# Optimization experiments

Measured on AMD Instinct MI355X. Metric: run time of the kernel, lower is better.

Reference implementation:

```python
import jax, jax.numpy as jnp
import numpy as np

B, T, F, U, H = 4096, 64, 128, 256, 256
MC_STEPS = 32
DENOISE = True


def setup_inputs() -> dict:
    key = jax.random.key(0)
    ks = jax.random.split(key, 12)
    su = 1.0 / np.sqrt(U)
    inp = {
        "x": jax.random.normal(ks[0], (B, T, F), jnp.float32),
        # LSTM params (torch gate order i,f,g,o)
        "W_ih": jax.random.uniform(ks[1], (4 * U, F), jnp.float32, -su, su),
        "W_hh": jax.random.uniform(ks[2], (4 * U, U), jnp.float32, -su, su),
        "b_ih": jax.random.uniform(ks[3], (4 * U,), jnp.float32, -su, su),
        "b_hh": jax.random.uniform(ks[4], (4 * U,), jnp.float32, -su, su),
        # CRBM conditioning nets: bias (ny), precision (ny), weights (ny*nh)
        "bias_W": jax.random.normal(ks[5], (F, U), jnp.float32) * su,
        "bias_b": jnp.zeros((F,), jnp.float32),
        "prec_W": jax.random.normal(ks[6], (F, U), jnp.float32) * su,
        "prec_b": jnp.zeros((F,), jnp.float32),
        "wts_W": jax.random.normal(ks[7], (F * H, U), jnp.float32) * su,
        "wts_b": jnp.zeros((F * H,), jnp.float32),
    }
    return inp


def _lstm_last_hidden(x, W_ih, W_hh, b_ih, b_hh):
    # single-layer batch_first LSTM; returns last hidden state [B, U]
    b, u = x.shape[0], W_hh.shape[1]
    bias = b_ih + b_hh

    def step(carry, xt):
        h, c = carry
        g = xt @ W_ih.T + h @ W_hh.T + bias          # [B, 4U]
        i, f, gg, o = jnp.split(g, 4, axis=-1)
        c = jax.nn.sigmoid(f) * c + jax.nn.sigmoid(i) * jnp.tanh(gg)
        h = jax.nn.sigmoid(o) * jnp.tanh(c)
        return (h, c), None

    h0 = jnp.zeros((b, u), x.dtype)
    (h, _), _ = jax.lax.scan(step, (h0, h0), jnp.swapaxes(x, 0, 1))
    return h


def _crbm_sample(xh, bias_W, bias_b, prec_W, prec_b, wts_W, wts_b,
                 mc_steps=MC_STEPS, denoise=DENOISE):
    b = xh.shape[0]
    bias = xh @ bias_W.T + bias_b                              # [B, F]
    precision = jax.nn.softplus(xh @ prec_W.T + prec_b) + 1e-6  # [B, F] > 0
    weights = (xh @ wts_W.T + wts_b).reshape(b, F, H)           # [B, F, H]
    std = jax.lax.rsqrt(precision)

    key = jax.random.key(1)
    k0, kloop = jax.random.split(key)
    y0 = bias + std * jax.random.normal(k0, bias.shape, bias.dtype)

    def gibbs(y, k):
        kh, ky = jax.random.split(k)
        h_prob = jax.nn.sigmoid(jnp.einsum("bf,bfh->bh", y, weights))
        h = (jax.random.uniform(kh, h_prob.shape) < h_prob).astype(y.dtype)
        mean = bias + jnp.einsum("bfh,bh->bf", weights, h) / precision
        y = mean + std * jax.random.normal(ky, mean.shape, mean.dtype)
        return y, mean

    y_last, means = jax.lax.scan(gibbs, y0, jax.random.split(kloop, mc_steps))
    y_model = means[-1] if denoise else y_last
    return y_model, bias, precision, weights


def reference(x, W_ih, W_hh, b_ih, b_hh, bias_W, bias_b, prec_W, prec_b, wts_W, wts_b):
    xh = _lstm_last_hidden(x, W_ih, W_hh, b_ih, b_hh)
    y_model, _, _, _ = _crbm_sample(xh, bias_W, bias_b, prec_W, prec_b, wts_W, wts_b)
    return y_model
```

## Files before the change

kernel.cpp:

```cpp
#include <hip/hip_runtime.h>
#include <stdint.h>

#pragma clang fp contract(off)

#define B 4096
#define T 64
#define F 128
#define U 256
#define H 256
#define GU 1024
#define NJ 32768
#define MC 32
#define CH 256
#define BT 32

__host__ __device__ inline void tf2x32(uint32_t k0, uint32_t k1,
                                       uint32_t x0, uint32_t x1,
                                       uint32_t& o0, uint32_t& o1) {
  uint32_t ks2 = k0 ^ k1 ^ 0x1BD11BDAu;
  x0 += k0; x1 += k1;
#define TFR(r) { x0 += x1; x1 = (x1 << r) | (x1 >> (32 - r)); x1 ^= x0; }
  TFR(13) TFR(15) TFR(26) TFR(6)
  x0 += k1;  x1 += ks2 + 1u;
  TFR(17) TFR(29) TFR(16) TFR(24)
  x0 += ks2; x1 += k0 + 2u;
  TFR(13) TFR(15) TFR(26) TFR(6)
  x0 += k0;  x1 += k1 + 3u;
  TFR(17) TFR(29) TFR(16) TFR(24)
  x0 += k1;  x1 += ks2 + 4u;
  TFR(13) TFR(15) TFR(26) TFR(6)
  x0 += ks2; x1 += k0 + 5u;
#undef TFR
  o0 = x0; o1 = x1;
}

__device__ inline uint32_t tf_bits(uint32_t kx, uint32_t ky, uint32_t i) {
  uint32_t o0, o1;
  tf2x32(kx, ky, 0u, i, o0, o1);
  return o0 ^ o1;
}

__device__ inline float u01_f32(uint32_t bits) {
  return __uint_as_float((bits >> 9) | 0x3F800000u) - 1.0f;
}

__device__ inline float erfinv_f32(float x) {
  float w = -log1pf(-(x * x));
  float p;
  if (w < 5.0f) {
    float ww = w - 2.5f;
    p = 2.81022636e-08f;
    p = p * ww + 3.43273939e-07f;
    p = p * ww + (-3.5233877e-06f);
    p = p * ww + (-4.39150654e-06f);
    p = p * ww + 0.00021858087f;
    p = p * ww + (-0.00125372503f);
    p = p * ww + (-0.00417768164f);
    p = p * ww + 0.246640727f;
    p = p * ww + 1.50140941f;
  } else {
    float ww = sqrtf(w) - 3.0f;
    p = -0.000200214257f;
    p = p * ww + 0.000100950558f;
    p = p * ww + 0.00134934322f;
    p = p * ww + (-0.00367342844f);
    p = p * ww + 0.00573950773f;
    p = p * ww + (-0.0076224613f);
    p = p * ww + 0.00943887047f;
    p = p * ww + 1.00167406f;
    p = p * ww + 2.83297682f;
  }
  return p * x;
}

__device__ inline float normal_f32(uint32_t kx, uint32_t ky, uint32_t i) {
  float f = u01_f32(tf_bits(kx, ky, i));
  const float lo = -0.99999994039535522461f;
  float v = f * 2.0f + lo;
  v = fmaxf(lo, v);
  return 1.4142135623730951f * erfinv_f32(v);
}

__device__ inline float sigmoid_f32(float x) {
  return 1.0f / (1.0f + expf(-x));
}
__device__ inline float softplus_f32(float x) {
  return fmaxf(x, 0.0f) + log1pf(expf(-fabsf(x)));
}

__global__ void prep_lstm_w_k(const float* __restrict__ W_ih, const float* __restrict__ W_hh,
                              const float* __restrict__ b_ih, const float* __restrict__ b_hh,
                              float4* __restrict__ w4t, float* __restrict__ biasg) {
  int idx = blockIdx.x * 256 + threadIdx.x;
  if (idx < GU * 96) {
    int j = idx / 96, k4 = idx - j * 96;
    float v[4];
#pragma unroll
    for (int m = 0; m < 4; ++m) {
      int k = k4 * 4 + m;
      v[m] = (k < F) ? W_ih[(size_t)j * F + k] : W_hh[(size_t)j * U + (k - F)];
    }
    w4t[(size_t)k4 * GU + j] = make_float4(v[0], v[1], v[2], v[3]);
  }
  if (idx < GU) biasg[idx] = b_ih[idx] + b_hh[idx];
}

__global__ void prep_wts_k(const float* __restrict__ wts_W, float4* __restrict__ wts4t) {
  int idx = blockIdx.x * 256 + threadIdx.x;
  if (idx >= NJ * 64) return;
  int j = idx >> 6, k4 = idx & 63;
  const float* r = wts_W + (size_t)j * U + k4 * 4;
  wts4t[(size_t)k4 * NJ + j] = make_float4(r[0], r[1], r[2], r[3]);
}

__global__ void prep_bp_k(const float* __restrict__ bias_W, const float* __restrict__ prec_W,
                          float4* __restrict__ bp4t) {
  int idx = blockIdx.x * 256 + threadIdx.x;
  if (idx >= 256 * 64) return;
  int j = idx >> 6, k4 = idx & 63;
  const float* r = (j < F) ? (bias_W + (size_t)j * U + k4 * 4)
                           : (prec_W + (size_t)(j - F) * U + k4 * 4);
  bp4t[(size_t)k4 * 256 + j] = make_float4(r[0], r[1], r[2], r[3]);
}

__global__ __launch_bounds__(256) void lstm_step_k(
    const float* __restrict__ x, const float* __restrict__ h_in,
    const float* __restrict__ c_in, const float4* __restrict__ w4t,
    const float* __restrict__ biasg, float* __restrict__ h_out,
    float* __restrict__ c_out, int t) {
  __shared__ __align__(16) float xt[BT * 128];
  __shared__ __align__(16) float ht[BT * 256];
  const int tid = threadIdx.x;
  const int b0 = blockIdx.x * BT;
  const int ut = blockIdx.y;
  for (int q = tid; q < BT * 32; q += 256) {
    int row = q >> 5, c4 = q & 31;
    *(float4*)(xt + row * 128 + c4 * 4) =
        *(const float4*)(x + ((size_t)(b0 + row) * T + t) * F + c4 * 4);
  }
  for (int q = tid; q < BT * 64; q += 256) {
    int row = q >> 6, c4 = q & 63;
    *(float4*)(ht + row * 256 + c4 * 4) =
        *(const float4*)(h_in + (size_t)(b0 + row) * U + c4 * 4);
  }
  __syncthreads();
  const int u_loc = tid & 63, bg = tid >> 6;
  const int u = ut * 64 + u_loc;
  float accX[4][8], accH[4][8];
#pragma unroll
  for (int g = 0; g < 4; ++g)
#pragma unroll
    for (int b = 0; b < 8; ++b) { accX[g][b] = 0.0f; accH[g][b] = 0.0f; }

#pragma unroll 4
  for (int k4 = 0; k4 < 32; ++k4) {
    float4 wf[4];
#pragma unroll
    for (int g = 0; g < 4; ++g) wf[g] = w4t[(size_t)k4 * GU + g * U + u];
#pragma unroll
    for (int b = 0; b < 8; ++b) {
      float4 av = *(const float4*)(xt + (bg * 8 + b) * 128 + k4 * 4);
#pragma unroll
      for (int g = 0; g < 4; ++g) {
        accX[g][b] = fmaf(av.x, wf[g].x, accX[g][b]);
        accX[g][b] = fmaf(av.y, wf[g].y, accX[g][b]);
        accX[g][b] = fmaf(av.z, wf[g].z, accX[g][b]);
        accX[g][b] = fmaf(av.w, wf[g].w, accX[g][b]);
      }
    }
  }
#pragma unroll 4
  for (int k4 = 32; k4 < 96; ++k4) {
    float4 wf[4];
#pragma unroll
    for (int g = 0; g < 4; ++g) wf[g] = w4t[(size_t)k4 * GU + g * U + u];
#pragma unroll
    for (int b = 0; b < 8; ++b) {
      float4 av = *(const float4*)(ht + (bg * 8 + b) * 256 + (k4 - 32) * 4);
#pragma unroll
      for (int g = 0; g < 4; ++g) {
        accH[g][b] = fmaf(av.x, wf[g].x, accH[g][b]);
        accH[g][b] = fmaf(av.y, wf[g].y, accH[g][b]);
        accH[g][b] = fmaf(av.z, wf[g].z, accH[g][b]);
        accH[g][b] = fmaf(av.w, wf[g].w, accH[g][b]);
      }
    }
  }
  float bi = biasg[u], bf = biasg[U + u], bgg = biasg[2 * U + u], bo = biasg[3 * U + u];
#pragma unroll
  for (int b = 0; b < 8; ++b) {
    size_t gi = (size_t)(b0 + bg * 8 + b) * U + u;
    float c = c_in[gi];
    float g_i = (accX[0][b] + accH[0][b]) + bi;
    float g_f = (accX[1][b] + accH[1][b]) + bf;
    float g_g = (accX[2][b] + accH[2][b]) + bgg;
    float g_o = (accX[3][b] + accH[3][b]) + bo;
    float t1 = sigmoid_f32(g_f) * c;
    float t2 = sigmoid_f32(g_i) * tanhf(g_g);
    float cn = t1 + t2;
    float hn = sigmoid_f32(g_o) * tanhf(cn);
    c_out[gi] = cn;
    h_out[gi] = hn;
  }
}

__global__ __launch_bounds__(256) void gemm_xh_k(
    const float* __restrict__ xh_c, const float4* __restrict__ wts4t,
    const float* __restrict__ wts_b, float* __restrict__ outp) {
  __shared__ __align__(16) float xl[64 * 256];
  const int tid = threadIdx.x;
  const int b0 = blockIdx.x * 64;
  const int j = blockIdx.y * 256 + tid;
  for (int q = tid; q < 64 * 64; q += 256) {
    int row = q >> 6, c4 = q & 63;
    *(float4*)(xl + row * 256 + c4 * 4) =
        *(const float4*)(xh_c + (size_t)(b0 + row) * U + c4 * 4);
  }
  __syncthreads();
  float acc[64];
#pragma unroll
  for (int b = 0; b < 64; ++b) acc[b] = 0.0f;
  for (int k4 = 0; k4 < 64; ++k4) {
    float4 wf = wts4t[(size_t)k4 * NJ + j];
#pragma unroll
    for (int b = 0; b < 64; ++b) {
      float4 av = *(const float4*)(xl + b * 256 + k4 * 4);
      acc[b] = fmaf(av.x, wf.x, acc[b]);
      acc[b] = fmaf(av.y, wf.y, acc[b]);
      acc[b] = fmaf(av.z, wf.z, acc[b]);
      acc[b] = fmaf(av.w, wf.w, acc[b]);
    }
  }
  float bb = wts_b[j];
#pragma unroll
  for (int b = 0; b < 64; ++b)
    outp[(size_t)(b0 + b) * NJ + j] = acc[b] + bb;
}

__global__ __launch_bounds__(256) void biasprec_k(
    const float* __restrict__ xh, const float4* __restrict__ bp4t,
    const float* __restrict__ bias_b, const float* __restrict__ prec_b,
    float* __restrict__ bias_g, float* __restrict__ prec_g) {
  __shared__ __align__(16) float xl[64 * 256];
  const int tid = threadIdx.x;
  const int b0 = blockIdx.x * 64;
  const int j = tid;
  for (int q = tid; q < 64 * 64; q += 256) {
    int row = q >> 6, c4 = q & 63;
    *(float4*)(xl + row * 256 + c4 * 4) =
        *(const float4*)(xh + (size_t)(b0 + row) * U + c4 * 4);
  }
  __syncthreads();
  float acc[64];
#pragma unroll
  for (int b = 0; b < 64; ++b) acc[b] = 0.0f;
  for (int k4 = 0; k4 < 64; ++k4) {
    float4 wf = bp4t[(size_t)k4 * 256 + j];
#pragma unroll
    for (int b = 0; b < 64; ++b) {
      float4 av = *(const float4*)(xl + b * 256 + k4 * 4);
      acc[b] = fmaf(av.x, wf.x, acc[b]);
      acc[b] = fmaf(av.y, wf.y, acc[b]);
      acc[b] = fmaf(av.z, wf.z, acc[b]);
      acc[b] = fmaf(av.w, wf.w, acc[b]);
    }
  }
  if (j < F) {
    float bb = bias_b[j];
#pragma unroll
    for (int b = 0; b < 64; ++b)
      bias_g[(size_t)(b0 + b) * F + j] = acc[b] + bb;
  } else {
    float pb = prec_b[j - F];
#pragma unroll
    for (int b = 0; b < 64; ++b)
      prec_g[(size_t)(b0 + b) * F + (j - F)] = softplus_f32(acc[b] + pb) + 1e-6f;
  }
}

struct GKeys {
  uint32_t k0x, k0y;
  uint32_t khx[32], khy[32], kyx[32], kyy[32];
};

__global__ __launch_bounds__(256) void gibbs_k(
    const float* __restrict__ w_g, const float* __restrict__ bias_g,
    const float* __restrict__ prec_g, float* __restrict__ outp, GKeys keys,
    int base) {
  __shared__ __align__(16) float wl[32768];
  __shared__ __align__(16) float yv[128];
  __shared__ __align__(16) float hv[256];
  __shared__ float bs[128];
  __shared__ float ps[128];
  __shared__ float ss[128];
  const int tid = threadIdx.x;
  const int bloc = blockIdx.x;
  const int gb = base + bloc;
  const float4* src = (const float4*)(w_g + (size_t)bloc * NJ);
  float4* wl4 = (float4*)wl;
  for (int q = tid; q < NJ / 4; q += 256) {
    int f = q >> 6;
    int j4 = q & 63;
    wl4[f * 64 + (j4 ^ (f & 7))] = src[q];
  }
  if (tid < F) {
    float bb = bias_g[(size_t)gb * F + tid];
    float pp = prec_g[(size_t)gb * F + tid];
    bs[tid] = bb; ps[tid] = pp;
    float sd = 1.0f / sqrtf(pp);
    ss[tid] = sd;
    float n = normal_f32(keys.k0x, keys.k0y, (uint32_t)(gb * F + tid));
    float t1 = sd * n;
    yv[tid] = bb + t1;
  }
  __syncthreads();
  for (int s_ = 0; s_ < MC; ++s_) {
    {
      const int j = tid;
      const int jq = j >> 2, jm = j & 3;
      float u = u01_f32(tf_bits(keys.khx[s_], keys.khy[s_], (uint32_t)(gb * H + j)));
      float acc = 0.0f;
#pragma unroll 4
      for (int fb = 0; fb < F; fb += 4) {
        float4 y4 = *(const float4*)(yv + fb);
        float w0 = wl[(fb + 0) * 256 + ((jq ^ ((fb + 0) & 7)) << 2) + jm];
        float w1 = wl[(fb + 1) * 256 + ((jq ^ ((fb + 1) & 7)) << 2) + jm];
        float w2 = wl[(fb + 2) * 256 + ((jq ^ ((fb + 2) & 7)) << 2) + jm];
        float w3 = wl[(fb + 3) * 256 + ((jq ^ ((fb + 3) & 7)) << 2) + jm];
        acc = fmaf(y4.x, w0, acc);
        acc = fmaf(y4.y, w1, acc);
        acc = fmaf(y4.z, w2, acc);
        acc = fmaf(y4.w, w3, acc);
      }
      float p = sigmoid_f32(acc);
      hv[j] = (u < p) ? 1.0f : 0.0f;
    }
    __syncthreads();
    if (tid < F) {
      const int sq = tid & 7;
      const float4* wr4 = wl4 + tid * 64;
      const float4* hv4 = (const float4*)hv;
      float n = 0.0f;
      if (s_ != MC - 1)
        n = normal_f32(keys.kyx[s_], keys.kyy[s_], (uint32_t)(gb * F + tid));
      float C0[8], C1[8], C2[8], C3[8];
#pragma unroll
      for (int l = 0; l < 8; ++l) { C0[l] = 0.0f; C1[l] = 0.0f; C2[l] = 0.0f; C3[l] = 0.0f; }
      for (int k = 0; k < 8; ++k) {
        int eq = k * 8;
        float4 wq[8], hq[8];
#pragma unroll
        for (int qq = 0; qq < 8; ++qq) {
          wq[qq] = wr4[(eq + qq) ^ sq];
          hq[qq] = hv4[eq + qq];
        }
        const float* wv = (const float*)wq;
        const float* hh = (const float*)hq;
#pragma unroll
        for (int l = 0; l < 8; ++l) {
          C0[l] = fmaf(wv[l],      hh[l],      C0[l]);
          C1[l] = fmaf(wv[8 + l],  hh[8 + l],  C1[l]);
          C2[l] = fmaf(wv[16 + l], hh[16 + l], C2[l]);
          C3[l] = fmaf(wv[24 + l], hh[24 + l], C3[l]);
        }
      }
      float L[8];
#pragma unroll
      for (int l = 0; l < 8; ++l) L[l] = (C0[l] + C1[l]) + (C2[l] + C3[l]);
      float S = ((L[0] + L[1]) + (L[2] + L[3])) + ((L[4] + L[5]) + (L[6] + L[7]));
      float d = S / ps[tid];
      float mean = bs[tid] + d;
      if (s_ == MC - 1) {
        outp[(size_t)gb * F + tid] = mean;
      } else {
        float t1 = ss[tid] * n;
        yv[tid] = mean + t1;
      }
    }
    __syncthreads();
  }
}

extern "C" void kernel_launch(void* const* d_in, const int* in_sizes, int n_in,
                              void* d_out, int out_size, void* d_ws, size_t ws_size,
                              hipStream_t stream) {
  const float* x      = (const float*)d_in[0];
  const float* W_ih   = (const float*)d_in[1];
  const float* W_hh   = (const float*)d_in[2];
  const float* b_ih   = (const float*)d_in[3];
  const float* b_hh   = (const float*)d_in[4];
  const float* bias_W = (const float*)d_in[5];
  const float* bias_b = (const float*)d_in[6];
  const float* prec_W = (const float*)d_in[7];
  const float* prec_b = (const float*)d_in[8];
  const float* wts_W  = (const float*)d_in[9];
  const float* wts_b  = (const float*)d_in[10];
  float* out = (float*)d_out;

  float* wsf = (float*)d_ws;
  size_t off = 0;
  float* w_g     = wsf + off; off += (size_t)CH * NJ;
  float* h_a     = wsf + off; off += (size_t)B * U;
  float* h_b     = wsf + off; off += (size_t)B * U;
  float* c_a     = wsf + off; off += (size_t)B * U;
  float* c_b     = wsf + off; off += (size_t)B * U;
  float* biasg_g = wsf + off; off += (size_t)B * F;
  float* precg_g = wsf + off; off += (size_t)B * F;
  float* w4t     = wsf + off; off += (size_t)96 * GU * 4;
  float* biasg   = wsf + off; off += GU;
  float* wts4t   = wsf + off; off += (size_t)64 * NJ * 4;
  float* bp4t    = wsf + off; off += (size_t)64 * 256 * 4;
  (void)ws_size;

  hipMemsetAsync(h_a, 0, (size_t)B * U * sizeof(float), stream);
  hipMemsetAsync(c_a, 0, (size_t)B * U * sizeof(float), stream);

  prep_lstm_w_k<<<(GU * 96 + 255) / 256, 256, 0, stream>>>(W_ih, W_hh, b_ih, b_hh,
                                                           (float4*)w4t, biasg);
  prep_wts_k<<<(NJ * 64) / 256, 256, 0, stream>>>(wts_W, (float4*)wts4t);
  prep_bp_k<<<(256 * 64) / 256, 256, 0, stream>>>(bias_W, prec_W, (float4*)bp4t);

  const float* hi = h_a; const float* ci = c_a;
  float* ho = h_b; float* co = c_b;
  for (int t = 0; t < T; ++t) {
    lstm_step_k<<<dim3(B / BT, 4), 256, 0, stream>>>(
        x, hi, ci, (const float4*)w4t, biasg, ho, co, t);
    const float* th_ = hi; hi = ho; ho = (float*)th_;
    const float* tc_ = ci; ci = co; co = (float*)tc_;
  }
  const float* xh = hi;

  biasprec_k<<<dim3(B / 64), 256, 0, stream>>>(xh, (const float4*)bp4t,
                                               bias_b, prec_b, biasg_g, precg_g);

  GKeys keys;
  uint32_t k0x, k0y, l0, l1;
  tf2x32(0u, 1u, 0u, 0u, k0x, k0y);
  tf2x32(0u, 1u, 0u, 1u, l0, l1);
  keys.k0x = k0x; keys.k0y = k0y;
  for (int s = 0; s < 32; ++s) {
    uint32_t ksx, ksy;
    tf2x32(l0, l1, 0u, (uint32_t)s, ksx, ksy);
    tf2x32(ksx, ksy, 0u, 0u, keys.khx[s], keys.khy[s]);
    tf2x32(ksx, ksy, 0u, 1u, keys.kyx[s], keys.kyy[s]);
  }

  for (int c = 0; c < B / CH; ++c) {
    gemm_xh_k<<<dim3(CH / 64, NJ / 256), 256, 0, stream>>>(
        xh + (size_t)c * CH * U, (const float4*)wts4t, wts_b, w_g);
    gibbs_k<<<dim3(CH), 256, 0, stream>>>(w_g, biasg_g, precg_g, out, keys, c * CH);
  }
}
```

Baseline: 7.884 ms.

## Retile weight GEMM, shrink biasprec tiles, widen gibbs blocks with nontemporal loads

The weights GEMM now gives each thread a 4-column by 16-row register tile instead of one column by 64 rows. That cuts the per-thread accumulator count and reuses each shared-memory activation load across four weight columns, and results are written with nontemporal stores. The bias/precision GEMM uses 16-row tiles with four times as many blocks, for more parallelism. The Gibbs kernel runs 512 threads per block: all of them stage the swizzled weight slab through registers with nontemporal loads, and only the first 256 run the sampling loop. This may leave half the threads idle during the Gibbs loop and change occupancy.

```diff
diff --git a/kernel.cpp b/kernel.cpp
--- a/kernel.cpp
+++ b/kernel.cpp
@@ -13,6 +13,8 @@
 #define MC 32
 #define CH 256
 #define BT 32
+
+typedef float nt_f4 __attribute__((ext_vector_type(4)));
 
 __host__ __device__ inline void tf2x32(uint32_t k0, uint32_t k1,
                                        uint32_t x0, uint32_t x1,
@@ -210,20 +212,69 @@
   __shared__ __align__(16) float xl[64 * 256];
   const int tid = threadIdx.x;
   const int b0 = blockIdx.x * 64;
-  const int j = blockIdx.y * 256 + tid;
+  const int jb = blockIdx.y * 256;
+  const int jl = tid & 63, bg = tid >> 6;
   for (int q = tid; q < 64 * 64; q += 256) {
     int row = q >> 6, c4 = q & 63;
     *(float4*)(xl + row * 256 + c4 * 4) =
         *(const float4*)(xh_c + (size_t)(b0 + row) * U + c4 * 4);
   }
   __syncthreads();
-  float acc[64];
-#pragma unroll
-  for (int b = 0; b < 64; ++b) acc[b] = 0.0f;
+  float acc[4][16];
+#pragma unroll
+  for (int q = 0; q < 4; ++q)
+#pragma unroll
+    for (int bb = 0; bb < 16; ++bb) acc[q][bb] = 0.0f;
+#pragma unroll 2
   for (int k4 = 0; k4 < 64; ++k4) {
-    float4 wf = wts4t[(size_t)k4 * NJ + j];
-#pragma unroll
-    for (int b = 0; b < 64; ++b) {
+    float4 wf[4];
+#pragma unroll
+    for (int q = 0; q < 4; ++q)
+      wf[q] = wts4t[(size_t)k4 * NJ + jb + q * 64 + jl];
+#pragma unroll
+    for (int bb = 0; bb < 16; ++bb) {
+      float4 av = *(const float4*)(xl + (bg * 16 + bb) * 256 + k4 * 4);
+#pragma unroll
+      for (int q = 0; q < 4; ++q) {
+        acc[q][bb] = fmaf(av.x, wf[q].x, acc[q][bb]);
+        acc[q][bb] = fmaf(av.y, wf[q].y, acc[q][bb]);
+        acc[q][bb] = fmaf(av.z, wf[q].z, acc[q][bb]);
+        acc[q][bb] = fmaf(av.w, wf[q].w, acc[q][bb]);
+      }
+    }
+  }
+#pragma unroll
+  for (int q = 0; q < 4; ++q) {
+    float bb_j = wts_b[jb + q * 64 + jl];
+#pragma unroll
+    for (int bb = 0; bb < 16; ++bb)
+      __builtin_nontemporal_store(acc[q][bb] + bb_j,
+          &outp[(size_t)(b0 + bg * 16 + bb) * NJ + jb + q * 64 + jl]);
+  }
+}
+
+__global__ __launch_bounds__(256) void biasprec_k(
+    const float* __restrict__ xh, const float4* __restrict__ bp4t,
+    const float* __restrict__ bias_b, const float* __restrict__ prec_b,
+    float* __restrict__ bias_g, float* __restrict__ prec_g) {
+  __shared__ __align__(16) float xl[16 * 256];
+  const int tid = threadIdx.x;
+  const int b0 = blockIdx.x * 16;
+  const int j = tid;
+  for (int q = tid; q < 16 * 64; q += 256) {
+    int row = q >> 6, c4 = q & 63;
+    *(float4*)(xl + row * 256 + c4 * 4) =
+        *(const float4*)(xh + (size_t)(b0 + row) * U + c4 * 4);
+  }
+  __syncthreads();
+  float acc[16];
+#pragma unroll
+  for (int b = 0; b < 16; ++b) acc[b] = 0.0f;
+#pragma unroll 2
+  for (int k4 = 0; k4 < 64; ++k4) {
+    float4 wf = bp4t[(size_t)k4 * 256 + j];
+#pragma unroll
+    for (int b = 0; b < 16; ++b) {
       float4 av = *(const float4*)(xl + b * 256 + k4 * 4);
       acc[b] = fmaf(av.x, wf.x, acc[b]);
       acc[b] = fmaf(av.y, wf.y, acc[b]);
@@ -231,49 +282,15 @@
       acc[b] = fmaf(av.w, wf.w, acc[b]);
     }
   }
-  float bb = wts_b[j];
-#pragma unroll
-  for (int b = 0; b < 64; ++b)
-    outp[(size_t)(b0 + b) * NJ + j] = acc[b] + bb;
-}
-
-__global__ __launch_bounds__(256) void biasprec_k(
-    const float* __restrict__ xh, const float4* __restrict__ bp4t,
-    const float* __restrict__ bias_b, const float* __restrict__ prec_b,
-    float* __restrict__ bias_g, float* __restrict__ prec_g) {
-  __shared__ __align__(16) float xl[64 * 256];
-  const int tid = threadIdx.x;
-  const int b0 = blockIdx.x * 64;
-  const int j = tid;
-  for (int q = tid; q < 64 * 64; q += 256) {
-    int row = q >> 6, c4 = q & 63;
-    *(float4*)(xl + row * 256 + c4 * 4) =
-        *(const float4*)(xh + (size_t)(b0 + row) * U + c4 * 4);
-  }
-  __syncthreads();
-  float acc[64];
-#pragma unroll
-  for (int b = 0; b < 64; ++b) acc[b] = 0.0f;
-  for (int k4 = 0; k4 < 64; ++k4) {
-    float4 wf = bp4t[(size_t)k4 * 256 + j];
-#pragma unroll
-    for (int b = 0; b < 64; ++b) {
-      float4 av = *(const float4*)(xl + b * 256 + k4 * 4);
-      acc[b] = fmaf(av.x, wf.x, acc[b]);
-      acc[b] = fmaf(av.y, wf.y, acc[b]);
-      acc[b] = fmaf(av.z, wf.z, acc[b]);
-      acc[b] = fmaf(av.w, wf.w, acc[b]);
-    }
-  }
   if (j < F) {
     float bb = bias_b[j];
 #pragma unroll
-    for (int b = 0; b < 64; ++b)
+    for (int b = 0; b < 16; ++b)
       bias_g[(size_t)(b0 + b) * F + j] = acc[b] + bb;
   } else {
     float pb = prec_b[j - F];
 #pragma unroll
-    for (int b = 0; b < 64; ++b)
+    for (int b = 0; b < 16; ++b)
       prec_g[(size_t)(b0 + b) * F + (j - F)] = softplus_f32(acc[b] + pb) + 1e-6f;
   }
 }
@@ -283,7 +300,7 @@
   uint32_t khx[32], khy[32], kyx[32], kyy[32];
 };
 
-__global__ __launch_bounds__(256) void gibbs_k(
+__global__ __launch_bounds__(512) void gibbs_k(
     const float* __restrict__ w_g, const float* __restrict__ bias_g,
     const float* __restrict__ prec_g, float* __restrict__ outp, GKeys keys,
     int base) {
@@ -296,12 +313,19 @@
   const int tid = threadIdx.x;
   const int bloc = blockIdx.x;
   const int gb = base + bloc;
-  const float4* src = (const float4*)(w_g + (size_t)bloc * NJ);
+  const nt_f4* src = (const nt_f4*)(w_g + (size_t)bloc * NJ);
   float4* wl4 = (float4*)wl;
-  for (int q = tid; q < NJ / 4; q += 256) {
-    int f = q >> 6;
-    int j4 = q & 63;
-    wl4[f * 64 + (j4 ^ (f & 7))] = src[q];
+  {
+    nt_f4 stg[16];
+#pragma unroll
+    for (int i = 0; i < 16; ++i) {
+      int p = tid + i * 512;
+      int f = p >> 6, j4 = p & 63;
+      stg[i] = __builtin_nontemporal_load(&src[f * 64 + (j4 ^ (f & 7))]);
+    }
+#pragma unroll
+    for (int i = 0; i < 16; ++i)
+      *(nt_f4*)(&wl4[tid + i * 512]) = stg[i];
   }
   if (tid < F) {
     float bb = bias_g[(size_t)gb * F + tid];
@@ -315,7 +339,7 @@
   }
   __syncthreads();
   for (int s_ = 0; s_ < MC; ++s_) {
-    {
+    if (tid < H) {
       const int j = tid;
       const int jq = j >> 2, jm = j & 3;
       float u = u01_f32(tf_bits(keys.khx[s_], keys.khy[s_], (uint32_t)(gb * H + j)));
@@ -412,8 +436,8 @@
   float* bp4t    = wsf + off; off += (size_t)64 * 256 * 4;
   (void)ws_size;
 
-  hipMemsetAsync(h_a, 0, (size_t)B * U * sizeof(float), stream);
-  hipMemsetAsync(c_a, 0, (size_t)B * U * sizeof(float), stream);
+  (void)hipMemsetAsync(h_a, 0, (size_t)B * U * sizeof(float), stream);
+  (void)hipMemsetAsync(c_a, 0, (size_t)B * U * sizeof(float), stream);
 
   prep_lstm_w_k<<<(GU * 96 + 255) / 256, 256, 0, stream>>>(W_ih, W_hh, b_ih, b_hh,
                                                            (float4*)w4t, biasg);
@@ -430,7 +454,7 @@
   }
   const float* xh = hi;
 
-  biasprec_k<<<dim3(B / 64), 256, 0, stream>>>(xh, (const float4*)bp4t,
+  biasprec_k<<<dim3(B / 16), 256, 0, stream>>>(xh, (const float4*)bp4t,
                                                bias_b, prec_b, biasg_g, precg_g);
 
   GKeys keys;
@@ -448,6 +472,6 @@
   for (int c = 0; c < B / CH; ++c) {
     gemm_xh_k<<<dim3(CH / 64, NJ / 256), 256, 0, stream>>>(
         xh + (size_t)c * CH * U, (const float4*)wts4t, wts_b, w_g);
-    gibbs_k<<<dim3(CH), 256, 0, stream>>>(w_g, biasg_g, precg_g, out, keys, c * CH);
-  }
-}
+    gibbs_k<<<dim3(CH), 512, 0, stream>>>(w_g, biasg_g, precg_g, out, keys, c * CH);
+  }
+}
```

Result: faster. 7.074 ms (-10.3%).
